# Kernel tuning notes

Measured on AMD Instinct MI355X. Metric: run time of the kernel, lower is better.

The kernel has to match this reference:

```python
import jax, jax.numpy as jnp
import numpy as np

N = 100000      # nodes
E = 1600000     # edges
NSG2 = 20000    # subgraph2 count
NSG = 2000      # subgraph count
NG = 64         # graphs
D = 64          # hidden dim
L = 5           # conv layers


def setup_inputs() -> dict:
    key = jax.random.key(0)
    ks = jax.random.split(key, 40)
    f = lambda i, shape: (jax.random.normal(ks[i], shape, jnp.float32) * 0.05)
    inp = {
        'z': jax.random.randint(ks[0], (N, 2), 0, 100),
        'edge_index': jax.random.randint(ks[1], (2, E), 0, N),
        'node_to_subgraph2': jax.random.randint(ks[2], (N,), 0, NSG2),
        'subgraph2_to_subgraph': jax.random.randint(ks[3], (NSG2,), 0, NSG),
        'subgraph_to_graph': jax.random.randint(ks[4], (NSG,), 0, NG),
        # learned params (stacked across the 5 layers where identical shape)
        'z_emb': f(5, (L, 100, D)),
        'trans_W': f(6, (L - 1, 2 * D, D)),  # transform_before_conv, layers 1..4
        'trans_b': f(7, (L - 1, D)),
        'conv_W': f(8, (L, D, D)),           # GatedGraphConv weight (num_layers=1)
        'gru_Wih': f(9, (L, D, 3 * D)),
        'gru_bih': f(10, (L, 3 * D)),
        'gru_Whh': f(11, (L, D, 3 * D)),
        'gru_bhh': f(12, (L, 3 * D)),
        'ep_W1': f(13, (D, D)), 'ep_b1': f(14, (D,)),
        'ep_W2': f(15, (D, D)), 'ep_b2': f(16, (D,)),
        'np_W1': f(17, (D, D)), 'np_b1': f(18, (D,)),
        'np_W2': f(19, (D, D)), 'np_b2': f(20, (D,)),
        'fc1_W': f(21, (D, 32)), 'fc1_b': f(22, (32,)),
        'fc2_W': f(23, (32, 16)), 'fc2_b': f(24, (16,)),
        'fc3_W': f(25, (16, 1)), 'fc3_b': f(26, (1,)),
    }
    return inp


def _gated_conv(x, src, dst, W, Wih, bih, Whh, bhh):
    # GatedGraphConv(out=64, num_layers=1): m = aggr_add(x_j @ W), x = GRUCell(m, x)
    h = x @ W                                            # [N, D]
    m = jax.ops.segment_sum(h[src], dst, num_segments=N)  # scatter-add messages
    gi = m @ Wih + bih                                   # [N, 3D]
    gh = x @ Whh + bhh
    ir, iz, inn = jnp.split(gi, 3, axis=-1)
    hr, hz, hn = jnp.split(gh, 3, axis=-1)
    r = jax.nn.sigmoid(ir + hr)
    zg = jax.nn.sigmoid(iz + hz)
    n = jnp.tanh(inn + r * hn)
    return (1.0 - zg) * n + zg * x


def reference(z, edge_index, node_to_subgraph2, subgraph2_to_subgraph, subgraph_to_graph,
              z_emb, trans_W, trans_b, conv_W, gru_Wih, gru_bih, gru_Whh, gru_bhh,
              ep_W1, ep_b1, ep_W2, ep_b2, np_W1, np_b1, np_W2, np_b2,
              fc1_W, fc1_b, fc2_W, fc2_b, fc3_W, fc3_b):
    src, dst = edge_index[0], edge_index[1]
    x = None
    for layer in range(L):
        ze = z_emb[layer][z].sum(axis=1)  # [N,2,D] -> [N,D]
        if x is None:
            x = ze
        else:
            x = jnp.concatenate([x, ze], axis=-1) @ trans_W[layer - 1] + trans_b[layer - 1]
        x = _gated_conv(x, src, dst, conv_W[layer], gru_Wih[layer], gru_bih[layer],
                        gru_Whh[layer], gru_bhh[layer])
    # 3-level add pooling with MLPs in between
    x = jax.ops.segment_sum(x, node_to_subgraph2, num_segments=NSG2)
    x = jax.nn.relu(x @ ep_W1 + ep_b1) @ ep_W2 + ep_b2
    x = jax.ops.segment_sum(x, subgraph2_to_subgraph, num_segments=NSG)
    x = jax.nn.relu(x @ np_W1 + np_b1) @ np_W2 + np_b2
    x = jax.ops.segment_sum(x, subgraph_to_graph, num_segments=NG)
    x = jax.nn.elu(x @ fc1_W + fc1_b)
    x = jax.nn.elu(x @ fc2_W + fc2_b)
    return x @ fc3_W + fc3_b  # [NG, 1]
```

## Files before the change

kernel.cpp:

```cpp
#include <hip/hip_runtime.h>
#include <hip/hip_bf16.h>

constexpr int N    = 100000;
constexpr int E    = 1600000;
constexpr int NSG2 = 20000;
constexpr int NSG  = 2000;
constexpr int NG   = 64;
constexpr int D    = 64;
constexpr int L    = 5;

constexpr int NPB   = 32;
constexpr int NBUCK = N / NPB;
constexpr int NSTR  = 8;
constexpr int SCAP  = 128;

typedef __attribute__((ext_vector_type(8))) short short8v;
typedef __attribute__((ext_vector_type(4))) float f32x4;

__device__ __forceinline__ float sigm(float x) { return 1.0f / (1.0f + expf(-x)); }
__device__ __forceinline__ float elu(float x)  { return x > 0.0f ? x : (expf(x) - 1.0f); }

__device__ __forceinline__ unsigned short f2b(float f) {
    union { float f; unsigned u; } x; x.f = f;
    unsigned r = (x.u + 0x7FFFu + ((x.u >> 16) & 1u)) >> 16;
    return (unsigned short)r;
}
__device__ __forceinline__ float b2f(unsigned short h) {
    union { unsigned u; float f; } x; x.u = (unsigned)h << 16;
    return x.f;
}

__global__ __launch_bounds__(256) void prep_kernel(const float* __restrict__ convW,
                                                   const float* __restrict__ Wih,
                                                   float* __restrict__ WihP) {
    int idx = blockIdx.x * 256 + threadIdx.x;
    if (idx >= L * 64 * 192) return;
    int l = idx / (64 * 192);
    int rem = idx % (64 * 192);
    int i = rem / 192, j = rem % 192;
    const float* W  = convW + l * 64 * 64;
    const float* Wi = Wih  + l * 64 * 192;
    float acc = 0.0f;
    for (int t = 0; t < 64; ++t) acc = fmaf(W[i * 64 + t], Wi[t * 192 + j], acc);
    WihP[idx] = acc;
}

__global__ __launch_bounds__(256) void packg_kernel(const float* __restrict__ WihP,
                                                    const float* __restrict__ gWhh,
                                                    unsigned short* __restrict__ Wgpk) {
    int idx = blockIdx.x * 256 + threadIdx.x;
    if (idx >= L * 2 * 12 * 2 * 64) return;
    int lane = idx & 63;
    int r1 = idx >> 6;
    int t  = r1 & 1;
    int r2 = r1 >> 1;
    int nt = r2 % 12;
    int lm = r2 / 12;
    int mat = lm & 1, l = lm >> 1;
    const float* W = mat ? (gWhh + (size_t)l * 64 * 192) : (WihP + (size_t)l * 64 * 192);
    int n  = nt * 16 + (lane & 15);
    int k0 = t * 32 + (lane >> 4) * 8;
    short8v v;
#pragma unroll
    for (int j = 0; j < 8; ++j) v[j] = (short)f2b(W[(k0 + j) * 192 + n]);
    *(short8v*)(Wgpk + (size_t)idx * 8) = v;
}

__global__ __launch_bounds__(256) void packt_kernel(const float* __restrict__ tW,
                                                    unsigned short* __restrict__ tWpk) {
    int idx = blockIdx.x * 256 + threadIdx.x;
    if (idx >= (L - 1) * 4 * 4 * 64) return;
    int lane = idx & 63;
    int r1 = idx >> 6;
    int t  = r1 & 3;
    int r2 = r1 >> 2;
    int nt = r2 & 3;
    int lm = r2 >> 2;
    const float* W = tW + (size_t)lm * 128 * 64;
    int n  = nt * 16 + (lane & 15);
    int k0 = t * 32 + (lane >> 4) * 8;
    short8v v;
#pragma unroll
    for (int j = 0; j < 8; ++j) v[j] = (short)f2b(W[(k0 + j) * 64 + n]);
    *(short8v*)(tWpk + (size_t)idx * 8) = v;
}

__global__ void bucketA_kernel(const int* __restrict__ src, const int* __restrict__ dst,
                               int* __restrict__ bcnt, unsigned* __restrict__ tmp) {
    int stripe = blockIdx.x & (NSTR - 1);
    for (int e = blockIdx.x * blockDim.x + threadIdx.x; e < E; e += gridDim.x * blockDim.x) {
        int d = dst[e];
        int cell = stripe * NBUCK + (d >> 5);
        int pos = atomicAdd(&bcnt[cell * 16], 1);
        if (pos < SCAP)
            tmp[(size_t)cell * SCAP + pos] = ((unsigned)(d & 31) << 17) | (unsigned)src[e];
    }
}

__global__ __launch_bounds__(1024) void bscan_kernel(const int* __restrict__ bcnt,
                                                     int* __restrict__ bbase,
                                                     int* __restrict__ rowptrN) {
    __shared__ int part[1024];
    int t = threadIdx.x;
    int loc[4]; int sum = 0;
#pragma unroll
    for (int j = 0; j < 4; ++j) {
        int b = t * 4 + j; int v = 0;
        if (b < NBUCK) {
#pragma unroll
            for (int s = 0; s < NSTR; ++s) v += min(bcnt[(s * NBUCK + b) * 16], SCAP);
        }
        loc[j] = v; sum += v;
    }
    part[t] = sum;
    __syncthreads();
    for (int off = 1; off < 1024; off <<= 1) {
        int u = (t >= off) ? part[t - off] : 0;
        __syncthreads();
        part[t] += u;
        __syncthreads();
    }
    int run = part[t] - sum;
#pragma unroll
    for (int j = 0; j < 4; ++j) {
        int b = t * 4 + j;
        if (b < NBUCK) bbase[b] = run;
        run += loc[j];
    }
    if (t == 1023) { bbase[NBUCK] = part[1023]; rowptrN[0] = part[1023]; }
}

__global__ __launch_bounds__(256) void bucketB_kernel(const unsigned* __restrict__ tmp,
                                                      const int* __restrict__ bcnt,
                                                      const int* __restrict__ bbase,
                                                      int* __restrict__ rowptr,
                                                      int* __restrict__ col) {
    __shared__ unsigned recs[NSTR * SCAP];
    __shared__ int scnt[NSTR];
    __shared__ int soff[NSTR + 1];
    __shared__ int cur[NPB];
    int b = blockIdx.x, tid = threadIdx.x;
    if (tid < NSTR) scnt[tid] = min(bcnt[(tid * NBUCK + b) * 16], SCAP);
    if (tid < NPB) cur[tid] = 0;
    __syncthreads();
    if (tid == 0) {
        int r = 0;
        for (int s = 0; s < NSTR; ++s) { soff[s] = r; r += scnt[s]; }
        soff[NSTR] = r;
    }
    __syncthreads();
    int total = soff[NSTR];
    for (int i = tid; i < NSTR * SCAP; i += 256) {
        int s = i >> 7, k = i & (SCAP - 1);
        if (k < scnt[s]) recs[soff[s] + k] = tmp[((size_t)s * NBUCK + b) * SCAP + k];
    }
    __syncthreads();
    for (int i = tid; i < total; i += 256) atomicAdd(&cur[recs[i] >> 17], 1);
    __syncthreads();
    if (tid == 0) {
        int base = bbase[b], r = 0;
        for (int j = 0; j < NPB; ++j) {
            int v = cur[j];
            cur[j] = base + r;
            rowptr[b * NPB + j] = base + r;
            r += v;
        }
    }
    __syncthreads();
    for (int i = tid; i < total; i += 256) {
        unsigned w = recs[i];
        int pos = atomicAdd(&cur[w >> 17], 1);
        col[pos] = (int)(w & 0x1FFFFu);
    }
}

__global__ __launch_bounds__(256) void embed_kernel(const int* __restrict__ z,
                                                    const float* __restrict__ zemb0,
                                                    float* __restrict__ x,
                                                    unsigned short* __restrict__ xb) {
    int idx = blockIdx.x * 256 + threadIdx.x;
    if (idx >= N * 16) return;
    int n = idx >> 4, k4 = idx & 15;
    float4 e0 = ((const float4*)(zemb0 + (size_t)z[n * 2] * 64))[k4];
    float4 e1 = ((const float4*)(zemb0 + (size_t)z[n * 2 + 1] * 64))[k4];
    float4 v; v.x = e0.x + e1.x; v.y = e0.y + e1.y; v.z = e0.z + e1.z; v.w = e0.w + e1.w;
    ((float4*)x)[idx] = v;
    ushort4 b; b.x = f2b(v.x); b.y = f2b(v.y); b.z = f2b(v.z); b.w = f2b(v.w);
    ((ushort4*)xb)[idx] = b;
}

template<int HAS_T>
__global__ __launch_bounds__(256) void fused_kernel(const unsigned short* __restrict__ xb_in,
                                                    float* __restrict__ xbuf,
                                                    unsigned short* __restrict__ xb_out,
                                                    const int* __restrict__ rowptr,
                                                    const int* __restrict__ col,
                                                    const unsigned short* __restrict__ Wgpk_l,
                                                    const float* __restrict__ bih,
                                                    const float* __restrict__ bhh,
                                                    const int* __restrict__ z,
                                                    const float* __restrict__ zemb_next,
                                                    const unsigned short* __restrict__ tWpk_next,
                                                    const float* __restrict__ tb_next) {
    __shared__ union {
        struct { unsigned short s[32][72]; unsigned short x[32][72]; } p1;
        unsigned short a[32][136];
    } u;
    int tid = threadIdx.x;
    int node0 = blockIdx.x * 32;
    int lane = tid & 63, w = tid >> 6;

    {
        int g8 = lane >> 3, cj = lane & 7;
        int nl = w * 8 + g8;
        int node = node0 + nl;
        float4 ownx = ((const float4*)(xb_in + (size_t)node * 64))[cj];
        int beg = rowptr[node], end = rowptr[node + 1];
        float a[8] = {};
        const unsigned short* __restrict__ xbc = xb_in + cj * 8;
        int i = beg;
        for (; i + 8 <= end; i += 8) {
            int u0 = col[i],     u1 = col[i + 1], u2 = col[i + 2], u3 = col[i + 3];
            int u4 = col[i + 4], u5 = col[i + 5], u6 = col[i + 6], u7 = col[i + 7];
            short8v v0 = *(const short8v*)(xbc + (size_t)u0 * 64);
            short8v v1 = *(const short8v*)(xbc + (size_t)u1 * 64);
            short8v v2 = *(const short8v*)(xbc + (size_t)u2 * 64);
            short8v v3 = *(const short8v*)(xbc + (size_t)u3 * 64);
            short8v v4 = *(const short8v*)(xbc + (size_t)u4 * 64);
            short8v v5 = *(const short8v*)(xbc + (size_t)u5 * 64);
            short8v v6 = *(const short8v*)(xbc + (size_t)u6 * 64);
            short8v v7 = *(const short8v*)(xbc + (size_t)u7 * 64);
#pragma unroll
            for (int j = 0; j < 8; ++j)
                a[j] += ((b2f((unsigned short)v0[j]) + b2f((unsigned short)v1[j])) +
                         (b2f((unsigned short)v2[j]) + b2f((unsigned short)v3[j]))) +
                        ((b2f((unsigned short)v4[j]) + b2f((unsigned short)v5[j])) +
                         (b2f((unsigned short)v6[j]) + b2f((unsigned short)v7[j])));
        }
        for (; i + 4 <= end; i += 4) {
            int u0 = col[i], u1 = col[i + 1], u2 = col[i + 2], u3 = col[i + 3];
            short8v v0 = *(const short8v*)(xbc + (size_t)u0 * 64);
            short8v v1 = *(const short8v*)(xbc + (size_t)u1 * 64);
            short8v v2 = *(const short8v*)(xbc + (size_t)u2 * 64);
            short8v v3 = *(const short8v*)(xbc + (size_t)u3 * 64);
#pragma unroll
            for (int j = 0; j < 8; ++j)
                a[j] += (b2f((unsigned short)v0[j]) + b2f((unsigned short)v1[j])) +
                        (b2f((unsigned short)v2[j]) + b2f((unsigned short)v3[j]));
        }
        for (; i + 2 <= end; i += 2) {
            int u0 = col[i], u1 = col[i + 1];
            short8v v0 = *(const short8v*)(xbc + (size_t)u0 * 64);
            short8v v1 = *(const short8v*)(xbc + (size_t)u1 * 64);
#pragma unroll
            for (int j = 0; j < 8; ++j)
                a[j] += b2f((unsigned short)v0[j]) + b2f((unsigned short)v1[j]);
        }
        if (i < end) {
            short8v v = *(const short8v*)(xbc + (size_t)col[i] * 64);
#pragma unroll
            for (int j = 0; j < 8; ++j) a[j] += b2f((unsigned short)v[j]);
        }
        short8v r;
#pragma unroll
        for (int j = 0; j < 8; ++j) r[j] = (short)f2b(a[j]);
        *(short8v*)&u.p1.s[nl][cj * 8] = r;
        *(float4*)&u.p1.x[nl][cj * 8] = ownx;
    }
    __syncthreads();

    int lr = lane & 15, lg = lane >> 4;
    short8v as_[2][2], ax_[2][2];
#pragma unroll
    for (int mt = 0; mt < 2; ++mt)
#pragma unroll
        for (int t = 0; t < 2; ++t) {
            int row = mt * 16 + lr, koff = t * 32 + lg * 8;
            as_[mt][t] = *(const short8v*)&u.p1.s[row][koff];
            ax_[mt][t] = *(const short8v*)&u.p1.x[row][koff];
        }
    if (HAS_T) __syncthreads();

    f32x4 accA[3][2] = {};
    f32x4 accB[3][2] = {};
#pragma unroll
    for (int g = 0; g < 3; ++g) {
        int nt = g * 4 + w;
#pragma unroll
        for (int t = 0; t < 2; ++t) {
            const unsigned short* pA = Wgpk_l + ((size_t)((0 * 12 + nt) * 2 + t) * 64 + lane) * 8;
            const unsigned short* pB = Wgpk_l + ((size_t)((1 * 12 + nt) * 2 + t) * 64 + lane) * 8;
            short8v bA = *(const short8v*)pA;
            short8v bB = *(const short8v*)pB;
#pragma unroll
            for (int mt = 0; mt < 2; ++mt) {
                accA[g][mt] = __builtin_amdgcn_mfma_f32_16x16x32_bf16(as_[mt][t], bA, accA[g][mt], 0, 0, 0);
                accB[g][mt] = __builtin_amdgcn_mfma_f32_16x16x32_bf16(ax_[mt][t], bB, accB[g][mt], 0, 0, 0);
            }
        }
    }

    int ch = w * 16 + lr;
    float bi0 = bih[ch], bi1 = bih[64 + ch], bi2 = bih[128 + ch];
    float bh0 = bhh[ch], bh1 = bhh[64 + ch], bh2 = bhh[128 + ch];
    float xo[2][4];
#pragma unroll
    for (int mt = 0; mt < 2; ++mt) {
#pragma unroll
        for (int reg = 0; reg < 4; ++reg) {
            int m = mt * 16 + lg * 4 + reg;
            float r  = sigm(accA[0][mt][reg] + bi0 + accB[0][mt][reg] + bh0);
            float zg = sigm(accA[1][mt][reg] + bi1 + accB[1][mt][reg] + bh1);
            float nn = tanhf(accA[2][mt][reg] + bi2 + r * (accB[2][mt][reg] + bh2));
            xo[mt][reg] = (1.0f - zg) * nn + zg * xbuf[(size_t)(node0 + m) * 64 + ch];
        }
    }

    if (HAS_T == 0) {
#pragma unroll
        for (int mt = 0; mt < 2; ++mt)
#pragma unroll
            for (int reg = 0; reg < 4; ++reg) {
                int m = mt * 16 + lg * 4 + reg;
                xbuf[(size_t)(node0 + m) * 64 + ch] = xo[mt][reg];
            }
        return;
    }

#pragma unroll
    for (int mt = 0; mt < 2; ++mt)
#pragma unroll
        for (int reg = 0; reg < 4; ++reg) {
            int m = mt * 16 + lg * 4 + reg;
            u.a[m][ch] = f2b(xo[mt][reg]);
        }
#pragma unroll
    for (int it = 0; it < 2; ++it) {
        int idx = it * 256 + tid;
        int n = idx >> 4, k4 = idx & 15;
        int z0 = z[(node0 + n) * 2], z1 = z[(node0 + n) * 2 + 1];
        float4 e0 = ((const float4*)(zemb_next + (size_t)z0 * 64))[k4];
        float4 e1 = ((const float4*)(zemb_next + (size_t)z1 * 64))[k4];
        ushort4 b;
        b.x = f2b(e0.x + e1.x); b.y = f2b(e0.y + e1.y);
        b.z = f2b(e0.z + e1.z); b.w = f2b(e0.w + e1.w);
        *(ushort4*)&u.a[n][64 + k4 * 4] = b;
    }
    __syncthreads();

    f32x4 tacc[2] = {};
#pragma unroll
    for (int t = 0; t < 4; ++t) {
        const unsigned short* pB = tWpk_next + ((size_t)(w * 4 + t) * 64 + lane) * 8;
        short8v bf = *(const short8v*)pB;
#pragma unroll
        for (int mt = 0; mt < 2; ++mt) {
            int row = mt * 16 + lr, koff = t * 32 + lg * 8;
            short8v af = *(const short8v*)&u.a[row][koff];
            tacc[mt] = __builtin_amdgcn_mfma_f32_16x16x32_bf16(af, bf, tacc[mt], 0, 0, 0);
        }
    }
    float tbc = tb_next[ch];
#pragma unroll
    for (int mt = 0; mt < 2; ++mt)
#pragma unroll
        for (int reg = 0; reg < 4; ++reg) {
            int m = mt * 16 + lg * 4 + reg;
            size_t o = (size_t)(node0 + m) * 64 + ch;
            float v = tacc[mt][reg] + tbc;
            xbuf[o] = v;
            xb_out[o] = f2b(v);
        }
}

__global__ void pool_kernel(const float* __restrict__ in, const int* __restrict__ idx,
                            float* __restrict__ out, int rows) {
    int i = blockIdx.x * 256 + threadIdx.x;
    if (i >= rows * 64) return;
    int r = i >> 6, c = i & 63;
    atomicAdd(out + (size_t)idx[r] * 64 + c, in[i]);
}

__global__ __launch_bounds__(256) void mlp_kernel(float* __restrict__ buf,
                                                  const float* __restrict__ W1,
                                                  const float* __restrict__ b1,
                                                  const float* __restrict__ W2,
                                                  const float* __restrict__ b2) {
    __shared__ float in_t[4][64];
    __shared__ float h_t[4][64];
    int tid = threadIdx.x;
    int c = tid & 63, r = tid >> 6;
    int row0 = blockIdx.x * 4;
    in_t[r][c] = buf[(size_t)(row0 + r) * 64 + c];
    __syncthreads();
    float acc = b1[c];
    for (int k = 0; k < 64; ++k) acc = fmaf(in_t[r][k], W1[k * 64 + c], acc);
    h_t[r][c] = fmaxf(acc, 0.0f);
    __syncthreads();
    acc = b2[c];
    for (int k = 0; k < 64; ++k) acc = fmaf(h_t[r][k], W2[k * 64 + c], acc);
    buf[(size_t)(row0 + r) * 64 + c] = acc;
}

__global__ __launch_bounds__(256) void final_kernel(const float* __restrict__ g,
                                                    const float* __restrict__ fc1W, const float* __restrict__ fc1b,
                                                    const float* __restrict__ fc2W, const float* __restrict__ fc2b,
                                                    const float* __restrict__ fc3W, const float* __restrict__ fc3b,
                                                    float* __restrict__ out) {
    __shared__ float gt[64][64];
    __shared__ float h1[64][32];
    __shared__ float h2[64][16];
    int tid = threadIdx.x;
    for (int i = tid; i < 64 * 64; i += 256) gt[i >> 6][i & 63] = g[i];
    __syncthreads();
    for (int i = tid; i < 64 * 32; i += 256) {
        int r = i >> 5, c = i & 31;
        float acc = fc1b[c];
        for (int k = 0; k < 64; ++k) acc = fmaf(gt[r][k], fc1W[k * 32 + c], acc);
        h1[r][c] = elu(acc);
    }
    __syncthreads();
    for (int i = tid; i < 64 * 16; i += 256) {
        int r = i >> 4, c = i & 15;
        float acc = fc2b[c];
        for (int k = 0; k < 32; ++k) acc = fmaf(h1[r][k], fc2W[k * 16 + c], acc);
        h2[r][c] = elu(acc);
    }
    __syncthreads();
    if (tid < 64) {
        float acc = fc3b[0];
        for (int k = 0; k < 16; ++k) acc = fmaf(h2[tid][k], fc3W[k], acc);
        out[tid] = acc;
    }
}

extern "C" void kernel_launch(void* const* d_in, const int* in_sizes, int n_in,
                              void* d_out, int out_size, void* d_ws, size_t ws_size,
                              hipStream_t stream) {
    const int*   z     = (const int*)d_in[0];
    const int*   ei    = (const int*)d_in[1];
    const int*   n2s2  = (const int*)d_in[2];
    const int*   s22s  = (const int*)d_in[3];
    const int*   s2g   = (const int*)d_in[4];
    const float* z_emb = (const float*)d_in[5];
    const float* tW    = (const float*)d_in[6];
    const float* tb    = (const float*)d_in[7];
    const float* convW = (const float*)d_in[8];
    const float* gWih  = (const float*)d_in[9];
    const float* gbih  = (const float*)d_in[10];
    const float* gWhh  = (const float*)d_in[11];
    const float* gbhh  = (const float*)d_in[12];
    const float* epW1  = (const float*)d_in[13];
    const float* epb1  = (const float*)d_in[14];
    const float* epW2  = (const float*)d_in[15];
    const float* epb2  = (const float*)d_in[16];
    const float* npW1  = (const float*)d_in[17];
    const float* npb1  = (const float*)d_in[18];
    const float* npW2  = (const float*)d_in[19];
    const float* npb2  = (const float*)d_in[20];
    const float* fc1W  = (const float*)d_in[21];
    const float* fc1b  = (const float*)d_in[22];
    const float* fc2W  = (const float*)d_in[23];
    const float* fc2b  = (const float*)d_in[24];
    const float* fc3W  = (const float*)d_in[25];
    const float* fc3b  = (const float*)d_in[26];

    const int* srcp = ei;
    const int* dstp = ei + E;

    float*          xbuf = (float*)d_ws;
    unsigned short* xbA  = (unsigned short*)(xbuf + (size_t)N * D);
    unsigned short* xbB  = xbA + (size_t)N * D;
    float*          WihP = (float*)(xbB + (size_t)N * D);
    int*            rowptr = (int*)(WihP + L * 64 * 192);
    int*            colbuf = rowptr + (N + 1);
    int*            bbase  = colbuf + E;
    uintptr_t pal = (uintptr_t)(bbase + NBUCK + 1);
    pal = (pal + 15) & ~(uintptr_t)15;
    unsigned short* Wgpk = (unsigned short*)pal;
    unsigned short* tWpk = Wgpk + (size_t)L * 2 * 12 * 2 * 64 * 8;
    unsigned* tmp  = (unsigned*)xbuf;
    int*      bcnt = (int*)(tmp + (size_t)NSTR * NBUCK * SCAP);
    float* sg2  = (float*)colbuf;
    float* sg   = sg2 + (size_t)NSG2 * D;
    float* gbuf = sg + (size_t)NSG * D;

    hipMemsetAsync(bcnt, 0, (size_t)NSTR * NBUCK * 16 * sizeof(int), stream);

    prep_kernel<<<(L * 64 * 192 + 255) / 256, 256, 0, stream>>>(convW, gWih, WihP);
    packg_kernel<<<(L * 2 * 12 * 2 * 64 + 255) / 256, 256, 0, stream>>>(WihP, gWhh, Wgpk);
    packt_kernel<<<((L - 1) * 4 * 4 * 64 + 255) / 256, 256, 0, stream>>>(tW, tWpk);

    bucketA_kernel<<<4096, 256, 0, stream>>>(srcp, dstp, bcnt, tmp);
    bscan_kernel<<<1, 1024, 0, stream>>>(bcnt, bbase, rowptr + N);
    bucketB_kernel<<<NBUCK, 256, 0, stream>>>(tmp, bcnt, bbase, rowptr, colbuf);

    embed_kernel<<<(N * 16 + 255) / 256, 256, 0, stream>>>(z, z_emb, xbuf, xbA);

    for (int l = 0; l < L; ++l) {
        const unsigned short* xin = (l & 1) ? xbB : xbA;
        unsigned short*       xout = (l & 1) ? xbA : xbB;
        if (l < L - 1) {
            fused_kernel<1><<<N / 32, 256, 0, stream>>>(
                xin, xbuf, xout, rowptr, colbuf,
                Wgpk + (size_t)l * 2 * 12 * 2 * 64 * 8,
                gbih + (size_t)l * 192, gbhh + (size_t)l * 192,
                z, z_emb + (size_t)(l + 1) * 100 * 64,
                tWpk + (size_t)l * 4 * 4 * 64 * 8, tb + (size_t)l * 64);
        } else {
            fused_kernel<0><<<N / 32, 256, 0, stream>>>(
                xin, xbuf, nullptr, rowptr, colbuf,
                Wgpk + (size_t)l * 2 * 12 * 2 * 64 * 8,
                gbih + (size_t)l * 192, gbhh + (size_t)l * 192,
                z, z_emb, tWpk, tb);
        }
    }

    hipMemsetAsync(sg2, 0, (size_t)(NSG2 + NSG + NG) * D * sizeof(float), stream);
    pool_kernel<<<(N * D + 255) / 256, 256, 0, stream>>>(xbuf, n2s2, sg2, N);
    mlp_kernel<<<NSG2 / 4, 256, 0, stream>>>(sg2, epW1, epb1, epW2, epb2);
    pool_kernel<<<(NSG2 * D + 255) / 256, 256, 0, stream>>>(sg2, s22s, sg, NSG2);
    mlp_kernel<<<NSG / 4, 256, 0, stream>>>(sg, npW1, npb1, npW2, npb2);
    pool_kernel<<<(NSG * D + 255) / 256, 256, 0, stream>>>(sg, s2g, gbuf, NSG);
    final_kernel<<<1, 256, 0, stream>>>(gbuf, fc1W, fc1b, fc2W, fc2b, fc3W, fc3b, (float*)d_out);
}
```

Before: 498.9 us.

## Drop fp32 state buffer, fuse first pooling into last layer, simplify CSR build

```diff
diff --git a/kernel.cpp b/kernel.cpp
--- a/kernel.cpp
+++ b/kernel.cpp
@@ -9,10 +9,9 @@
 constexpr int D    = 64;
 constexpr int L    = 5;
 
-constexpr int NPB   = 32;
-constexpr int NBUCK = N / NPB;
+constexpr int CB    = (N + 255) / 256;
 constexpr int NSTR  = 8;
-constexpr int SCAP  = 128;
+constexpr int SCAP2 = 768;
 
 typedef __attribute__((ext_vector_type(8))) short short8v;
 typedef __attribute__((ext_vector_type(4))) float f32x4;
@@ -85,113 +84,88 @@
     *(short8v*)(tWpk + (size_t)idx * 8) = v;
 }
 
-__global__ void bucketA_kernel(const int* __restrict__ src, const int* __restrict__ dst,
-                               int* __restrict__ bcnt, unsigned* __restrict__ tmp) {
+__global__ void csrA_kernel(const int* __restrict__ src, const int* __restrict__ dst,
+                            int* __restrict__ bcnt, unsigned* __restrict__ tmp) {
     int stripe = blockIdx.x & (NSTR - 1);
     for (int e = blockIdx.x * blockDim.x + threadIdx.x; e < E; e += gridDim.x * blockDim.x) {
         int d = dst[e];
-        int cell = stripe * NBUCK + (d >> 5);
+        int cell = stripe * CB + (d >> 8);
         int pos = atomicAdd(&bcnt[cell * 16], 1);
-        if (pos < SCAP)
-            tmp[(size_t)cell * SCAP + pos] = ((unsigned)(d & 31) << 17) | (unsigned)src[e];
-    }
-}
-
-__global__ __launch_bounds__(1024) void bscan_kernel(const int* __restrict__ bcnt,
-                                                     int* __restrict__ bbase,
-                                                     int* __restrict__ rowptrN) {
-    __shared__ int part[1024];
-    int t = threadIdx.x;
-    int loc[4]; int sum = 0;
-#pragma unroll
-    for (int j = 0; j < 4; ++j) {
-        int b = t * 4 + j; int v = 0;
-        if (b < NBUCK) {
-#pragma unroll
-            for (int s = 0; s < NSTR; ++s) v += min(bcnt[(s * NBUCK + b) * 16], SCAP);
-        }
-        loc[j] = v; sum += v;
-    }
-    part[t] = sum;
-    __syncthreads();
-    for (int off = 1; off < 1024; off <<= 1) {
-        int u = (t >= off) ? part[t - off] : 0;
+        if (pos < SCAP2)
+            tmp[(size_t)cell * SCAP2 + pos] = ((unsigned)(d & 255) << 17) | (unsigned)src[e];
+    }
+}
+
+__global__ __launch_bounds__(256) void csrB_kernel(const unsigned* __restrict__ tmp,
+                                                   const int* __restrict__ bcnt,
+                                                   int* __restrict__ rowptr,
+                                                   int* __restrict__ col) {
+    __shared__ int hist[256];
+    __shared__ int scanb[256];
+    __shared__ int cur[256];
+    __shared__ int scnt[NSTR];
+    __shared__ int red[4];
+    int b = blockIdx.x, t = threadIdx.x;
+    int lane = t & 63, wid = t >> 6;
+
+    int myb = 0;
+    for (int cb = t; cb < b; cb += 256) {
+        int tot = 0;
+#pragma unroll
+        for (int s = 0; s < NSTR; ++s) tot += min(bcnt[(s * CB + cb) * 16], SCAP2);
+        myb += tot;
+    }
+#pragma unroll
+    for (int off = 32; off > 0; off >>= 1) myb += __shfl_down(myb, off, 64);
+    if (lane == 0) red[wid] = myb;
+    if (t < NSTR) scnt[t] = min(bcnt[(t * CB + b) * 16], SCAP2);
+    hist[t] = 0;
+    __syncthreads();
+    int base = red[0] + red[1] + red[2] + red[3];
+
+    for (int s = 0; s < NSTR; ++s)
+        for (int i = t; i < scnt[s]; i += 256)
+            atomicAdd(&hist[tmp[((size_t)s * CB + b) * SCAP2 + i] >> 17], 1);
+    __syncthreads();
+
+    scanb[t] = hist[t];
+    __syncthreads();
+    for (int off = 1; off < 256; off <<= 1) {
+        int v = (t >= off) ? scanb[t - off] : 0;
         __syncthreads();
-        part[t] += u;
+        scanb[t] += v;
         __syncthreads();
     }
-    int run = part[t] - sum;
-#pragma unroll
-    for (int j = 0; j < 4; ++j) {
-        int b = t * 4 + j;
-        if (b < NBUCK) bbase[b] = run;
-        run += loc[j];
-    }
-    if (t == 1023) { bbase[NBUCK] = part[1023]; rowptrN[0] = part[1023]; }
-}
-
-__global__ __launch_bounds__(256) void bucketB_kernel(const unsigned* __restrict__ tmp,
-                                                      const int* __restrict__ bcnt,
-                                                      const int* __restrict__ bbase,
-                                                      int* __restrict__ rowptr,
-                                                      int* __restrict__ col) {
-    __shared__ unsigned recs[NSTR * SCAP];
-    __shared__ int scnt[NSTR];
-    __shared__ int soff[NSTR + 1];
-    __shared__ int cur[NPB];
-    int b = blockIdx.x, tid = threadIdx.x;
-    if (tid < NSTR) scnt[tid] = min(bcnt[(tid * NBUCK + b) * 16], SCAP);
-    if (tid < NPB) cur[tid] = 0;
-    __syncthreads();
-    if (tid == 0) {
-        int r = 0;
-        for (int s = 0; s < NSTR; ++s) { soff[s] = r; r += scnt[s]; }
-        soff[NSTR] = r;
-    }
-    __syncthreads();
-    int total = soff[NSTR];
-    for (int i = tid; i < NSTR * SCAP; i += 256) {
-        int s = i >> 7, k = i & (SCAP - 1);
-        if (k < scnt[s]) recs[soff[s] + k] = tmp[((size_t)s * NBUCK + b) * SCAP + k];
-    }
-    __syncthreads();
-    for (int i = tid; i < total; i += 256) atomicAdd(&cur[recs[i] >> 17], 1);
-    __syncthreads();
-    if (tid == 0) {
-        int base = bbase[b], r = 0;
-        for (int j = 0; j < NPB; ++j) {
-            int v = cur[j];
-            cur[j] = base + r;
-            rowptr[b * NPB + j] = base + r;
-            r += v;
-        }
-    }
-    __syncthreads();
-    for (int i = tid; i < total; i += 256) {
-        unsigned w = recs[i];
-        int pos = atomicAdd(&cur[w >> 17], 1);
-        col[pos] = (int)(w & 0x1FFFFu);
-    }
+    int excl = scanb[t] - hist[t];
+    int node = b * 256 + t;
+    if (node < N) rowptr[node] = base + excl;
+    if (b == CB - 1 && t == 255) rowptr[N] = base + scanb[255];
+    cur[t] = base + excl;
+    __syncthreads();
+
+    for (int s = 0; s < NSTR; ++s)
+        for (int i = t; i < scnt[s]; i += 256) {
+            unsigned rec = tmp[((size_t)s * CB + b) * SCAP2 + i];
+            int pos = atomicAdd(&cur[rec >> 17], 1);
+            col[pos] = (int)(rec & 0x1FFFFu);
+        }
 }
 
 __global__ __launch_bounds__(256) void embed_kernel(const int* __restrict__ z,
                                                     const float* __restrict__ zemb0,
-                                                    float* __restrict__ x,
                                                     unsigned short* __restrict__ xb) {
     int idx = blockIdx.x * 256 + threadIdx.x;
     if (idx >= N * 16) return;
     int n = idx >> 4, k4 = idx & 15;
     float4 e0 = ((const float4*)(zemb0 + (size_t)z[n * 2] * 64))[k4];
     float4 e1 = ((const float4*)(zemb0 + (size_t)z[n * 2 + 1] * 64))[k4];
-    float4 v; v.x = e0.x + e1.x; v.y = e0.y + e1.y; v.z = e0.z + e1.z; v.w = e0.w + e1.w;
-    ((float4*)x)[idx] = v;
-    ushort4 b; b.x = f2b(v.x); b.y = f2b(v.y); b.z = f2b(v.z); b.w = f2b(v.w);
+    ushort4 b; b.x = f2b(e0.x + e1.x); b.y = f2b(e0.y + e1.y);
+    b.z = f2b(e0.z + e1.z); b.w = f2b(e0.w + e1.w);
     ((ushort4*)xb)[idx] = b;
 }
 
 template<int HAS_T>
 __global__ __launch_bounds__(256) void fused_kernel(const unsigned short* __restrict__ xb_in,
-                                                    float* __restrict__ xbuf,
                                                     unsigned short* __restrict__ xb_out,
                                                     const int* __restrict__ rowptr,
                                                     const int* __restrict__ col,
@@ -201,7 +175,9 @@
                                                     const int* __restrict__ z,
                                                     const float* __restrict__ zemb_next,
                                                     const unsigned short* __restrict__ tWpk_next,
-                                                    const float* __restrict__ tb_next) {
+                                                    const float* __restrict__ tb_next,
+                                                    const int* __restrict__ n2s2,
+                                                    float* __restrict__ sg2) {
     __shared__ union {
         struct { unsigned short s[32][72]; unsigned short x[32][72]; } p1;
         unsigned short a[32][136];
@@ -270,6 +246,7 @@
     __syncthreads();
 
     int lr = lane & 15, lg = lane >> 4;
+    int ch = w * 16 + lr;
     short8v as_[2][2], ax_[2][2];
 #pragma unroll
     for (int mt = 0; mt < 2; ++mt)
@@ -279,6 +256,12 @@
             as_[mt][t] = *(const short8v*)&u.p1.s[row][koff];
             ax_[mt][t] = *(const short8v*)&u.p1.x[row][koff];
         }
+    float xres[2][4];
+#pragma unroll
+    for (int mt = 0; mt < 2; ++mt)
+#pragma unroll
+        for (int reg = 0; reg < 4; ++reg)
+            xres[mt][reg] = b2f(u.p1.x[mt * 16 + lg * 4 + reg][ch]);
     if (HAS_T) __syncthreads();
 
     f32x4 accA[3][2] = {};
@@ -300,7 +283,6 @@
         }
     }
 
-    int ch = w * 16 + lr;
     float bi0 = bih[ch], bi1 = bih[64 + ch], bi2 = bih[128 + ch];
     float bh0 = bhh[ch], bh1 = bhh[64 + ch], bh2 = bhh[128 + ch];
     float xo[2][4];
@@ -308,11 +290,10 @@
     for (int mt = 0; mt < 2; ++mt) {
 #pragma unroll
         for (int reg = 0; reg < 4; ++reg) {
-            int m = mt * 16 + lg * 4 + reg;
             float r  = sigm(accA[0][mt][reg] + bi0 + accB[0][mt][reg] + bh0);
             float zg = sigm(accA[1][mt][reg] + bi1 + accB[1][mt][reg] + bh1);
             float nn = tanhf(accA[2][mt][reg] + bi2 + r * (accB[2][mt][reg] + bh2));
-            xo[mt][reg] = (1.0f - zg) * nn + zg * xbuf[(size_t)(node0 + m) * 64 + ch];
+            xo[mt][reg] = (1.0f - zg) * nn + zg * xres[mt][reg];
         }
     }
 
@@ -322,7 +303,7 @@
 #pragma unroll
             for (int reg = 0; reg < 4; ++reg) {
                 int m = mt * 16 + lg * 4 + reg;
-                xbuf[(size_t)(node0 + m) * 64 + ch] = xo[mt][reg];
+                atomicAdd(&sg2[(size_t)n2s2[node0 + m] * 64 + ch], xo[mt][reg]);
             }
         return;
     }
@@ -366,10 +347,7 @@
 #pragma unroll
         for (int reg = 0; reg < 4; ++reg) {
             int m = mt * 16 + lg * 4 + reg;
-            size_t o = (size_t)(node0 + m) * 64 + ch;
-            float v = tacc[mt][reg] + tbc;
-            xbuf[o] = v;
-            xb_out[o] = f2b(v);
+            xb_out[(size_t)(node0 + m) * 64 + ch] = f2b(tacc[mt][reg] + tbc);
         }
 }
 
@@ -468,56 +446,56 @@
     const int* srcp = ei;
     const int* dstp = ei + E;
 
-    float*          xbuf = (float*)d_ws;
-    unsigned short* xbA  = (unsigned short*)(xbuf + (size_t)N * D);
-    unsigned short* xbB  = xbA + (size_t)N * D;
+    unsigned short* xbA = (unsigned short*)d_ws;
+    unsigned short* xbB = xbA + (size_t)N * D;
     float*          WihP = (float*)(xbB + (size_t)N * D);
     int*            rowptr = (int*)(WihP + L * 64 * 192);
     int*            colbuf = rowptr + (N + 1);
-    int*            bbase  = colbuf + E;
-    uintptr_t pal = (uintptr_t)(bbase + NBUCK + 1);
+    uintptr_t pal = (uintptr_t)(colbuf + E);
     pal = (pal + 15) & ~(uintptr_t)15;
     unsigned short* Wgpk = (unsigned short*)pal;
     unsigned short* tWpk = Wgpk + (size_t)L * 2 * 12 * 2 * 64 * 8;
-    unsigned* tmp  = (unsigned*)xbuf;
-    int*      bcnt = (int*)(tmp + (size_t)NSTR * NBUCK * SCAP);
-    float* sg2  = (float*)colbuf;
-    float* sg   = sg2 + (size_t)NSG2 * D;
-    float* gbuf = sg + (size_t)NSG * D;
-
-    hipMemsetAsync(bcnt, 0, (size_t)NSTR * NBUCK * 16 * sizeof(int), stream);
+    uintptr_t pal2 = (uintptr_t)(tWpk + (size_t)(L - 1) * 4 * 4 * 64 * 8);
+    pal2 = (pal2 + 15) & ~(uintptr_t)15;
+    unsigned* tmp  = (unsigned*)pal2;
+    int*      bcnt = (int*)(tmp + (size_t)CB * NSTR * SCAP2);
+    float*    sg2  = (float*)(bcnt + (size_t)CB * NSTR * 16);
+    float*    sg   = sg2 + (size_t)NSG2 * D;
+    float*    gbuf = sg + (size_t)NSG * D;
+
+    hipMemsetAsync(bcnt, 0, (size_t)CB * NSTR * 16 * sizeof(int), stream);
+    hipMemsetAsync(sg2, 0, (size_t)(NSG2 + NSG + NG) * D * sizeof(float), stream);
 
     prep_kernel<<<(L * 64 * 192 + 255) / 256, 256, 0, stream>>>(convW, gWih, WihP);
     packg_kernel<<<(L * 2 * 12 * 2 * 64 + 255) / 256, 256, 0, stream>>>(WihP, gWhh, Wgpk);
     packt_kernel<<<((L - 1) * 4 * 4 * 64 + 255) / 256, 256, 0, stream>>>(tW, tWpk);
 
-    bucketA_kernel<<<4096, 256, 0, stream>>>(srcp, dstp, bcnt, tmp);
-    bscan_kernel<<<1, 1024, 0, stream>>>(bcnt, bbase, rowptr + N);
-    bucketB_kernel<<<NBUCK, 256, 0, stream>>>(tmp, bcnt, bbase, rowptr, colbuf);
-
-    embed_kernel<<<(N * 16 + 255) / 256, 256, 0, stream>>>(z, z_emb, xbuf, xbA);
+    csrA_kernel<<<4096, 256, 0, stream>>>(srcp, dstp, bcnt, tmp);
+    csrB_kernel<<<CB, 256, 0, stream>>>(tmp, bcnt, rowptr, colbuf);
+
+    embed_kernel<<<(N * 16 + 255) / 256, 256, 0, stream>>>(z, z_emb, xbA);
 
     for (int l = 0; l < L; ++l) {
         const unsigned short* xin = (l & 1) ? xbB : xbA;
         unsigned short*       xout = (l & 1) ? xbA : xbB;
         if (l < L - 1) {
             fused_kernel<1><<<N / 32, 256, 0, stream>>>(
-                xin, xbuf, xout, rowptr, colbuf,
+                xin, xout, rowptr, colbuf,
                 Wgpk + (size_t)l * 2 * 12 * 2 * 64 * 8,
                 gbih + (size_t)l * 192, gbhh + (size_t)l * 192,
                 z, z_emb + (size_t)(l + 1) * 100 * 64,
-                tWpk + (size_t)l * 4 * 4 * 64 * 8, tb + (size_t)l * 64);
+                tWpk + (size_t)l * 4 * 4 * 64 * 8, tb + (size_t)l * 64,
+                nullptr, nullptr);
         } else {
             fused_kernel<0><<<N / 32, 256, 0, stream>>>(
-                xin, xbuf, nullptr, rowptr, colbuf,
+                xin, nullptr, rowptr, colbuf,
                 Wgpk + (size_t)l * 2 * 12 * 2 * 64 * 8,
                 gbih + (size_t)l * 192, gbhh + (size_t)l * 192,
-                z, z_emb, tWpk, tb);
-        }
-    }
-
-    hipMemsetAsync(sg2, 0, (size_t)(NSG2 + NSG + NG) * D * sizeof(float), stream);
-    pool_kernel<<<(N * D + 255) / 256, 256, 0, stream>>>(xbuf, n2s2, sg2, N);
+                z, z_emb, tWpk, tb,
+                n2s2, sg2);
+        }
+    }
+
     mlp_kernel<<<NSG2 / 4, 256, 0, stream>>>(sg2, epW1, epb1, epW2, epb2);
     pool_kernel<<<(NSG2 * D + 255) / 256, 256, 0, stream>>>(sg2, s22s, sg, NSG2);
     mlp_kernel<<<NSG / 4, 256, 0, stream>>>(sg, npW1, npb1, npW2, npb2);
```

Result: faster. 466.4 us (-6.5%).
